# Kernel optimization log

Measured on AMD Instinct MI355X. Metric: run time of the kernel, lower is better.

The kernel has to match this reference:

```python
import jax, jax.numpy as jnp
import numpy as np

D_QK = 64

def _xavier(key, shape):
    # matches nn.init.xavier_uniform_ on (H, fan_in, fan_out)
    fan_in, fan_out = shape[-2], shape[-1]
    limit = float(np.sqrt(6.0 / (fan_in + fan_out)))
    return jax.random.uniform(key, shape, jnp.float32, -limit, limit)

def setup_inputs() -> dict:
    key = jax.random.key(0)
    kx, kq, kk, kv = jax.random.split(key, 4)
    B, M, d_model, H, d_QK, d_V = 4, 2048, 1024, 16, 64, 64
    x = jax.random.normal(kx, (B, M, d_model), jnp.float32)
    W_Q = _xavier(kq, (H, d_model, d_QK))
    W_K = _xavier(kk, (H, d_model, d_QK))
    W_V = _xavier(kv, (H, d_model, d_V))
    return {"x": x, "W_Q": W_Q, "W_K": W_K, "W_V": W_V}

def reference(x, W_Q, W_K, W_V):
    B, M, N = x.shape
    H = W_Q.shape[0]
    # per-head projections: [B,H,M,d]
    Q = jnp.einsum('bmn,hnd->bhmd', x, W_Q)
    K = jnp.einsum('bmn,hnd->bhmd', x, W_K)
    V = jnp.einsum('bmn,hnd->bhmd', x, W_V)
    scale = 1.0 / jnp.sqrt(jnp.asarray(D_QK, x.dtype))
    attn = jax.nn.softmax(jnp.einsum('bhmd,bhkd->bhmk', Q, K) * scale, axis=-1)
    out = jnp.einsum('bhmk,bhkd->bhmd', attn, V)  # [B,H,M,d_V]
    # transpose heads next to d_V and concat: [B,M,H*d_V] == [B,M,N]
    return out.transpose(0, 2, 1, 3).reshape(B, M, N)
```

## Files before the change

### kernel.cpp

```cpp
#include <hip/hip_runtime.h>

typedef __attribute__((ext_vector_type(8))) _Float16 f16x8;
typedef __attribute__((ext_vector_type(2))) __fp16 fp16v2;
typedef __attribute__((ext_vector_type(4))) float f32x4;
typedef _Float16 f16;
typedef unsigned short u16;
typedef unsigned int u32;

#define DEV __device__ __forceinline__

DEV u32 packh2(float a, float b) {
  union { f16 h[2]; u32 u; } x;
  x.h[0] = (f16)a; x.h[1] = (f16)b;
  return x.u;
}
DEV u32 pkrtz(float a, float b) {
  union { fp16v2 h; u32 u; } x;
  x.h = __builtin_amdgcn_cvt_pkrtz(a, b);
  return x.u;
}
DEV float exp2_fast(float x) {
  float r;
  asm("v_exp_f32 %0, %1" : "=v"(r) : "v"(x));
  return r;
}

typedef __attribute__((address_space(1))) const u32 ASG_u32;
typedef __attribute__((address_space(3))) u32 ASL_u32;
DEV void gload16(const void* g, void* l) {
  __builtin_amdgcn_global_load_lds((ASG_u32*)g, (ASL_u32*)l, 16, 0, 0);
}

__global__ __launch_bounds__(256) void k_half_x(const float* __restrict__ x,
                                                f16* __restrict__ xh) {
  const size_t i = ((size_t)blockIdx.x * 256 + threadIdx.x) * 8;
  float4 a = *(const float4*)(x + i);
  float4 c = *(const float4*)(x + i + 4);
  uint4 u;
  u.x = packh2(a.x, a.y); u.y = packh2(a.z, a.w);
  u.z = packh2(c.x, c.y); u.w = packh2(c.z, c.w);
  *(uint4*)(xh + i) = u;
}

__global__ __launch_bounds__(256) void k_prep_w(const float* __restrict__ Wq,
                                                const float* __restrict__ Wk,
                                                const float* __restrict__ Wv,
                                                f16* __restrict__ wt) {
  __shared__ float tile[64][65];
  const int bx = blockIdx.x;
  const int w = bx >> 8;
  const int rem = bx & 255;
  const int h = rem >> 4;
  const int nc = rem & 15;
  const float* W = (w == 0) ? Wq : ((w == 1) ? Wk : Wv);
  const int t = threadIdx.x;

  {
    const int r = t >> 2;
    const int cc = (t & 3) * 16;
    const float* src = W + ((size_t)h * 1024 + nc * 64 + r) * 64 + cc;
#pragma unroll
    for (int j = 0; j < 4; ++j) {
      float4 v = *(const float4*)(src + j * 4);
      tile[r][cc + j * 4 + 0] = v.x;
      tile[r][cc + j * 4 + 1] = v.y;
      tile[r][cc + j * 4 + 2] = v.z;
      tile[r][cc + j * 4 + 3] = v.w;
    }
  }
  __syncthreads();
  {
    const int d = t >> 2;
    const int n0 = (t & 3) * 16;
    const size_t base = ((size_t)(w * 16 + h) * 64 + d) * 1024 + nc * 64 + n0;
    uint4 u0, u1;
    u0.x = packh2(tile[n0 + 0][d], tile[n0 + 1][d]);
    u0.y = packh2(tile[n0 + 2][d], tile[n0 + 3][d]);
    u0.z = packh2(tile[n0 + 4][d], tile[n0 + 5][d]);
    u0.w = packh2(tile[n0 + 6][d], tile[n0 + 7][d]);
    u1.x = packh2(tile[n0 + 8][d], tile[n0 + 9][d]);
    u1.y = packh2(tile[n0 + 10][d], tile[n0 + 11][d]);
    u1.z = packh2(tile[n0 + 12][d], tile[n0 + 13][d]);
    u1.w = packh2(tile[n0 + 14][d], tile[n0 + 15][d]);
    *(uint4*)(wt + base) = u0;
    *(uint4*)(wt + base + 8) = u1;
  }
}

__global__ __launch_bounds__(256, 4) void k_proj(
    const f16* __restrict__ xh, const f16* __restrict__ wt,
    f16* __restrict__ Q, f16* __restrict__ K, f16* __restrict__ Vt) {
  __shared__ __align__(16) char ldsb[24576];
  int bid = blockIdx.x;
  bid = (bid & 7) * 384 + (bid >> 3);
  const int bm = bid / 48;
  const int bn = bid % 48;
  const int w = bn >> 4;
  const int h = bn & 15;
  const bool isV = (w == 2);
  const int t = threadIdx.x;
  const int wave = t >> 6;
  const int lane = t & 63;
  const int wr = wave >> 1;
  const int wc = wave & 1;

  f32x4 acc[4][2];
#pragma unroll
  for (int mi = 0; mi < 4; ++mi)
#pragma unroll
    for (int ni = 0; ni < 2; ++ni) acc[mi][ni] = (f32x4)(0.0f);

  for (int kt = 0; kt < 16; ++kt) {
    const int k0 = kt * 64;
#pragma unroll
    for (int i = 0; i < 4; ++i) {
      const int ci = wave * 4 + i;
      const int row = ci * 8 + (lane >> 3);
      const int cb = ((lane & 7) * 16) ^ ((row & 7) << 4);
      const size_t gb = ((size_t)(bm * 128 + row) * 1024 + k0) * 2;
      gload16((const char*)xh + gb + cb, ldsb + ci * 1024);
    }
#pragma unroll
    for (int i = 0; i < 2; ++i) {
      const int ci = wave * 2 + i;
      const int row = ci * 8 + (lane >> 3);
      const int cb = ((lane & 7) * 16) ^ ((row & 7) << 4);
      const size_t gb = ((size_t)(bn * 64 + row) * 1024 + k0) * 2;
      gload16((const char*)wt + gb + cb, ldsb + 16384 + ci * 1024);
    }
    __syncthreads();

#pragma unroll
    for (int ks = 0; ks < 2; ++ks) {
      f16x8 af[4], bfr[2];
#pragma unroll
      for (int mi = 0; mi < 4; ++mi) {
        const int row = wr * 64 + mi * 16 + (lane & 15);
        const int cb = (((lane >> 4) * 16) + ks * 64) ^ ((row & 7) << 4);
        af[mi] = *(const f16x8*)(ldsb + row * 128 + cb);
      }
#pragma unroll
      for (int ni = 0; ni < 2; ++ni) {
        const int row = wc * 32 + ni * 16 + (lane & 15);
        const int cb = (((lane >> 4) * 16) + ks * 64) ^ ((row & 7) << 4);
        bfr[ni] = *(const f16x8*)(ldsb + 16384 + row * 128 + cb);
      }
#pragma unroll
      for (int mi = 0; mi < 4; ++mi)
#pragma unroll
        for (int ni = 0; ni < 2; ++ni)
          acc[mi][ni] = __builtin_amdgcn_mfma_f32_16x16x32_f16(af[mi], bfr[ni], acc[mi][ni], 0, 0, 0);
    }
    __syncthreads();
  }

  const int rb = bm * 128 + wr * 64;
#pragma unroll
  for (int mi = 0; mi < 4; ++mi) {
#pragma unroll
    for (int ni = 0; ni < 2; ++ni) {
      f32x4 v = acc[mi][ni];
      const int d = wc * 32 + ni * 16 + (lane & 15);
      const int m0 = rb + mi * 16 + ((lane >> 4) << 2);
      const int b = m0 >> 11;
      const int ml = m0 & 2047;
      if (isV) {
        uint2 u;
        u.x = packh2(v[0], v[1]);
        u.y = packh2(v[2], v[3]);
        *(uint2*)(Vt + ((size_t)((b * 16 + h) * 64 + d)) * 2048 + ml) = u;
      } else {
        const float sc = (w == 0) ? 0.18033688f : 1.0f;
        f16* A = (w == 0) ? Q : K;
#pragma unroll
        for (int j = 0; j < 4; ++j)
          A[((size_t)(b * 16 + h) * 2048 + (ml + j)) * 64 + d] = (f16)(v[j] * sc);
      }
    }
  }
}

__global__ __launch_bounds__(256, 3) void k_attn(
    const f16* __restrict__ Q, const f16* __restrict__ K,
    const f16* __restrict__ Vt, float* __restrict__ out) {
  __shared__ __align__(16) char ldsb[49152];
  int bid = blockIdx.x;
  bid = (bid & 7) * 128 + (bid >> 3);
  const int bh = bid >> 4;
  const int qt = bid & 15;
  const int b = bh >> 4;
  const int h = bh & 15;
  const int t = threadIdx.x;
  const int wave = t >> 6;
  const int lane = t & 63;
  const int l15 = lane & 15;
  const int g = lane >> 4;
  char* sP = ldsb + 32768 + wave * 4096;

  f16x8 qf[2][2];
  const size_t qbase = ((size_t)bh * 2048 + qt * 128 + wave * 32) * 64;
#pragma unroll
  for (int mf = 0; mf < 2; ++mf)
#pragma unroll
    for (int ks = 0; ks < 2; ++ks) {
      const size_t off = qbase + (size_t)(mf * 16 + l15) * 64 + ks * 32 + g * 8;
      qf[mf][ks] = *(const f16x8*)(Q + off);
    }

  f32x4 o[2][4];
  float ms[2], ls[2];
#pragma unroll
  for (int mf = 0; mf < 2; ++mf) { ms[mf] = -1e30f; ls[mf] = 0.0f; }
#pragma unroll
  for (int mf = 0; mf < 2; ++mf)
#pragma unroll
    for (int df = 0; df < 4; ++df) o[mf][df] = (f32x4)(0.0f);

  const size_t kvbase = (size_t)bh * 2048 * 64;

  const int srow = (wave * 2) * 8 + (lane >> 3);
  const int scb0 = ((lane & 7) * 16) ^ ((srow & 7) << 4);

#pragma unroll 1
  for (int kt = 0; kt < 33; ++kt) {
    if (kt < 32) {
      char* dst = ldsb + (kt & 1) * 16384;
#pragma unroll
      for (int i = 0; i < 2; ++i) {
        const int ci = wave * 2 + i;
        const int row = srow + i * 8;
        const size_t gk = (kvbase + (size_t)(kt * 64 + row) * 64) * 2;
        gload16((const char*)K + gk + scb0, dst + ci * 1024);
        const size_t gv = (kvbase + (size_t)row * 2048 + kt * 64) * 2;
        gload16((const char*)Vt + gv + scb0, dst + 8192 + ci * 1024);
      }
    }
    if (kt == 0) { __syncthreads(); continue; }
    const char* kb = ldsb + ((kt - 1) & 1) * 16384;
    const char* vbuf = kb + 8192;

    f32x4 st[2][4];
#pragma unroll
    for (int mf = 0; mf < 2; ++mf)
#pragma unroll
      for (int nf = 0; nf < 4; ++nf) st[mf][nf] = (f32x4)(0.0f);
#pragma unroll
    for (int ks = 0; ks < 2; ++ks) {
      f16x8 kf[4];
#pragma unroll
      for (int nf = 0; nf < 4; ++nf) {
        const int row = nf * 16 + l15;
        const int cb = ((g * 16) + ks * 64) ^ ((row & 7) << 4);
        kf[nf] = *(const f16x8*)(kb + row * 128 + cb);
      }
#pragma unroll
      for (int mf = 0; mf < 2; ++mf)
#pragma unroll
        for (int nf = 0; nf < 4; ++nf)
          st[mf][nf] = __builtin_amdgcn_mfma_f32_16x16x32_f16(kf[nf], qf[mf][ks], st[mf][nf], 0, 0, 0);
    }

#pragma unroll
    for (int mf = 0; mf < 2; ++mf) {
      float rm = fmaxf(fmaxf(fmaxf(st[mf][0][0], st[mf][0][1]), fmaxf(st[mf][0][2], st[mf][0][3])),
                       fmaxf(fmaxf(st[mf][1][0], st[mf][1][1]), fmaxf(st[mf][1][2], st[mf][1][3])));
      rm = fmaxf(rm, fmaxf(fmaxf(fmaxf(st[mf][2][0], st[mf][2][1]), fmaxf(st[mf][2][2], st[mf][2][3])),
                           fmaxf(fmaxf(st[mf][3][0], st[mf][3][1]), fmaxf(st[mf][3][2], st[mf][3][3]))));
      rm = fmaxf(rm, __shfl_xor(rm, 16));
      rm = fmaxf(rm, __shfl_xor(rm, 32));
      if (__any(rm > ms[mf] + 11.5f)) {
        const float mnew = fmaxf(ms[mf], rm);
        const float alpha = exp2_fast(ms[mf] - mnew);
        ms[mf] = mnew;
        ls[mf] *= alpha;
        f32x4 av;
#pragma unroll
        for (int j = 0; j < 4; ++j) av[j] = __shfl(alpha, g * 4 + j);
#pragma unroll
        for (int df = 0; df < 4; ++df) o[mf][df] *= av;
      }
      const float m = ms[mf];
      float p[4][4], part = 0.0f;
#pragma unroll
      for (int nf = 0; nf < 4; ++nf) {
#pragma unroll
        for (int j = 0; j < 4; ++j) {
          p[nf][j] = exp2_fast(st[mf][nf][j] - m);
          part += p[nf][j];
        }
      }
      ls[mf] += part;
      const int prow = mf * 16 + l15;
      char* pr = sP + prow * 128;
      const int swz = (prow & 7) << 4;
#pragma unroll
      for (int nf = 0; nf < 4; ++nf) {
        uint2 u;
        u.x = pkrtz(p[nf][0], p[nf][1]);
        u.y = pkrtz(p[nf][2], p[nf][3]);
        *(uint2*)(pr + (((nf << 5) + (g << 3)) ^ swz)) = u;
      }
    }
    asm volatile("" ::: "memory");

#pragma unroll
    for (int ks = 0; ks < 2; ++ks) {
      f16x8 pa[2];
#pragma unroll
      for (int mf = 0; mf < 2; ++mf) {
        const int prow = mf * 16 + l15;
        pa[mf] = *(const f16x8*)(sP + prow * 128 + ((ks * 64 + g * 16) ^ ((prow & 7) << 4)));
      }
#pragma unroll
      for (int df = 0; df < 4; ++df) {
        const int row = df * 16 + l15;
        const int cb = ((g * 16) + ks * 64) ^ ((row & 7) << 4);
        const f16x8 vb = *(const f16x8*)(vbuf + row * 128 + cb);
#pragma unroll
        for (int mf = 0; mf < 2; ++mf)
          o[mf][df] = __builtin_amdgcn_mfma_f32_16x16x32_f16(pa[mf], vb, o[mf][df], 0, 0, 0);
      }
    }
    __syncthreads();
  }

#pragma unroll
  for (int mf = 0; mf < 2; ++mf) {
    float l = ls[mf];
    l += __shfl_xor(l, 16);
    l += __shfl_xor(l, 32);
    const float inv = 1.0f / l;
    f32x4 iv;
#pragma unroll
    for (int j = 0; j < 4; ++j) iv[j] = __shfl(inv, g * 4 + j);
#pragma unroll
    for (int j = 0; j < 4; ++j) {
      const int m = qt * 128 + wave * 32 + mf * 16 + g * 4 + j;
#pragma unroll
      for (int df = 0; df < 4; ++df) {
        const int d = df * 16 + l15;
        out[((size_t)(b * 2048 + m)) * 1024 + h * 64 + d] = o[mf][df][j] * iv[j];
      }
    }
  }
}

extern "C" void kernel_launch(void* const* d_in, const int* in_sizes, int n_in,
                              void* d_out, int out_size, void* d_ws, size_t ws_size,
                              hipStream_t stream) {
  (void)in_sizes; (void)n_in; (void)out_size; (void)ws_size;
  const float* x  = (const float*)d_in[0];
  const float* Wq = (const float*)d_in[1];
  const float* Wk = (const float*)d_in[2];
  const float* Wv = (const float*)d_in[3];
  float* out = (float*)d_out;

  f16* ws = (f16*)d_ws;
  f16* xh = ws + 0;
  f16* wt = ws + 8388608;
  f16* Q  = ws + 11534336;
  f16* K  = ws + 19922944;
  f16* Vt = ws + 28311552;

  k_half_x<<<4096, 256, 0, stream>>>(x, xh);
  k_prep_w<<<768, 256, 0, stream>>>(Wq, Wk, Wv, wt);
  k_proj<<<3072, 256, 0, stream>>>(xh, wt, Q, K, Vt);
  k_attn<<<1024, 256, 0, stream>>>(Q, K, Vt, out);
}
```

Baseline: 194.7 us.

## Fold running max into MFMA init, halve P scratch, raise occupancy and prioritize MFMA

QK^T accumulators are now initialised to -m, so the running-max subtraction happens inside the MFMA. That removes the per-element subtract from the common no-rescale path. The per-wave P staging buffer shrinks to one 16-row tile that is reused per mf, which cuts LDS from 48KB to 40KB, and launch bounds go from 3 to 4 blocks per CU. s_setprio brackets the MFMA sections to favour matrix issue across waves. The risks are higher register pressure under the tighter occupancy target, extra LDS round-trips per mf, and a changed initial max of 0 that relies on the lazy-rescale threshold for numerical safety.

Result: slower. 216.1 us (+11.0%).

```diff
diff --git a/kernel.cpp b/kernel.cpp
--- a/kernel.cpp
+++ b/kernel.cpp
@@ -180,10 +180,10 @@
   }
 }
 
-__global__ __launch_bounds__(256, 3) void k_attn(
+__global__ __launch_bounds__(256, 4) void k_attn(
     const f16* __restrict__ Q, const f16* __restrict__ K,
     const f16* __restrict__ Vt, float* __restrict__ out) {
-  __shared__ __align__(16) char ldsb[49152];
+  __shared__ __align__(16) char ldsb[40960];
   int bid = blockIdx.x;
   bid = (bid & 7) * 128 + (bid >> 3);
   const int bh = bid >> 4;
@@ -195,7 +195,7 @@
   const int lane = t & 63;
   const int l15 = lane & 15;
   const int g = lane >> 4;
-  char* sP = ldsb + 32768 + wave * 4096;
+  char* sP = ldsb + 32768 + wave * 2048;
 
   f16x8 qf[2][2];
   const size_t qbase = ((size_t)bh * 2048 + qt * 128 + wave * 32) * 64;
@@ -208,9 +208,7 @@
     }
 
   f32x4 o[2][4];
-  float ms[2], ls[2];
-#pragma unroll
-  for (int mf = 0; mf < 2; ++mf) { ms[mf] = -1e30f; ls[mf] = 0.0f; }
+  float ms[2] = {0.0f, 0.0f}, ls[2] = {0.0f, 0.0f};
 #pragma unroll
   for (int mf = 0; mf < 2; ++mf)
 #pragma unroll
@@ -243,7 +241,8 @@
 #pragma unroll
     for (int mf = 0; mf < 2; ++mf)
 #pragma unroll
-      for (int nf = 0; nf < 4; ++nf) st[mf][nf] = (f32x4)(0.0f);
+      for (int nf = 0; nf < 4; ++nf) st[mf][nf] = (f32x4)(-ms[mf]);
+    __builtin_amdgcn_s_setprio(1);
 #pragma unroll
     for (int ks = 0; ks < 2; ++ks) {
       f16x8 kf[4];
@@ -259,40 +258,52 @@
         for (int nf = 0; nf < 4; ++nf)
           st[mf][nf] = __builtin_amdgcn_mfma_f32_16x16x32_f16(kf[nf], qf[mf][ks], st[mf][nf], 0, 0, 0);
     }
-
+    __builtin_amdgcn_s_setprio(0);
+
+    f16x8 pa[2][2];
 #pragma unroll
     for (int mf = 0; mf < 2; ++mf) {
-      float rm = fmaxf(fmaxf(fmaxf(st[mf][0][0], st[mf][0][1]), fmaxf(st[mf][0][2], st[mf][0][3])),
-                       fmaxf(fmaxf(st[mf][1][0], st[mf][1][1]), fmaxf(st[mf][1][2], st[mf][1][3])));
-      rm = fmaxf(rm, fmaxf(fmaxf(fmaxf(st[mf][2][0], st[mf][2][1]), fmaxf(st[mf][2][2], st[mf][2][3])),
-                           fmaxf(fmaxf(st[mf][3][0], st[mf][3][1]), fmaxf(st[mf][3][2], st[mf][3][3]))));
+      float ra = fmaxf(fmaxf(st[mf][0][0], st[mf][0][1]), st[mf][0][2]);
+      ra = fmaxf(fmaxf(ra, st[mf][0][3]), st[mf][1][0]);
+      ra = fmaxf(fmaxf(ra, st[mf][1][1]), st[mf][1][2]);
+      ra = fmaxf(ra, st[mf][1][3]);
+      float rb2 = fmaxf(fmaxf(st[mf][2][0], st[mf][2][1]), st[mf][2][2]);
+      rb2 = fmaxf(fmaxf(rb2, st[mf][2][3]), st[mf][3][0]);
+      rb2 = fmaxf(fmaxf(rb2, st[mf][3][1]), st[mf][3][2]);
+      rb2 = fmaxf(rb2, st[mf][3][3]);
+      float rm = fmaxf(ra, rb2);
       rm = fmaxf(rm, __shfl_xor(rm, 16));
       rm = fmaxf(rm, __shfl_xor(rm, 32));
-      if (__any(rm > ms[mf] + 11.5f)) {
-        const float mnew = fmaxf(ms[mf], rm);
-        const float alpha = exp2_fast(ms[mf] - mnew);
-        ms[mf] = mnew;
+      float p[4][4], part = 0.0f;
+      if (__any(rm > 11.5f)) {
+        const float rmp = fmaxf(rm, 0.0f);
+        const float alpha = exp2_fast(-rmp);
+        ms[mf] += rmp;
         ls[mf] *= alpha;
         f32x4 av;
 #pragma unroll
         for (int j = 0; j < 4; ++j) av[j] = __shfl(alpha, g * 4 + j);
 #pragma unroll
         for (int df = 0; df < 4; ++df) o[mf][df] *= av;
-      }
-      const float m = ms[mf];
-      float p[4][4], part = 0.0f;
-#pragma unroll
-      for (int nf = 0; nf < 4; ++nf) {
-#pragma unroll
-        for (int j = 0; j < 4; ++j) {
-          p[nf][j] = exp2_fast(st[mf][nf][j] - m);
-          part += p[nf][j];
-        }
+#pragma unroll
+        for (int nf = 0; nf < 4; ++nf)
+#pragma unroll
+          for (int j = 0; j < 4; ++j) {
+            p[nf][j] = exp2_fast(st[mf][nf][j] - rmp);
+            part += p[nf][j];
+          }
+      } else {
+#pragma unroll
+        for (int nf = 0; nf < 4; ++nf)
+#pragma unroll
+          for (int j = 0; j < 4; ++j) {
+            p[nf][j] = exp2_fast(st[mf][nf][j]);
+            part += p[nf][j];
+          }
       }
       ls[mf] += part;
-      const int prow = mf * 16 + l15;
-      char* pr = sP + prow * 128;
-      const int swz = (prow & 7) << 4;
+      char* pr = sP + l15 * 128;
+      const int swz = (l15 & 7) << 4;
 #pragma unroll
       for (int nf = 0; nf < 4; ++nf) {
         uint2 u;
@@ -300,17 +311,16 @@
         u.y = pkrtz(p[nf][2], p[nf][3]);
         *(uint2*)(pr + (((nf << 5) + (g << 3)) ^ swz)) = u;
       }
-    }
-    asm volatile("" ::: "memory");
-
+      asm volatile("" ::: "memory");
+#pragma unroll
+      for (int ks = 0; ks < 2; ++ks)
+        pa[mf][ks] = *(const f16x8*)(pr + ((ks * 64 + g * 16) ^ swz));
+      asm volatile("" ::: "memory");
+    }
+
+    __builtin_amdgcn_s_setprio(1);
 #pragma unroll
     for (int ks = 0; ks < 2; ++ks) {
-      f16x8 pa[2];
-#pragma unroll
-      for (int mf = 0; mf < 2; ++mf) {
-        const int prow = mf * 16 + l15;
-        pa[mf] = *(const f16x8*)(sP + prow * 128 + ((ks * 64 + g * 16) ^ ((prow & 7) << 4)));
-      }
 #pragma unroll
       for (int df = 0; df < 4; ++df) {
         const int row = df * 16 + l15;
@@ -318,9 +328,10 @@
         const f16x8 vb = *(const f16x8*)(vbuf + row * 128 + cb);
 #pragma unroll
         for (int mf = 0; mf < 2; ++mf)
-          o[mf][df] = __builtin_amdgcn_mfma_f32_16x16x32_f16(pa[mf], vb, o[mf][df], 0, 0, 0);
-      }
-    }
+          o[mf][df] = __builtin_amdgcn_mfma_f32_16x16x32_f16(pa[mf][ks], vb, o[mf][df], 0, 0, 0);
+      }
+    }
+    __builtin_amdgcn_s_setprio(0);
     __syncthreads();
   }
 
```
